# Performance work log

Hardware: AMD Instinct MI355X
Metric: run time of the kernel (lower is better)

Reference implementation:

```python
import jax, jax.numpy as jnp
import numpy as np

N_NODES = 100000
N_EDGES = 1600000
IN_CH, HID_CH, OUT_CH = 128, 128, 64


def _glorot(key, shape):
    lim = np.sqrt(6.0 / (shape[0] + shape[1])).astype(np.float32)
    return jax.random.uniform(key, shape, jnp.float32, -lim, lim)


def setup_inputs() -> dict:
    key = jax.random.key(0)
    ks = jax.random.split(key, 11)
    x = jax.random.normal(ks[0], (N_NODES, IN_CH), jnp.float32)
    edge_index = jax.random.randint(ks[1], (2, N_EDGES), 0, N_NODES, dtype=jnp.int64)
    dims = [(IN_CH, HID_CH), (HID_CH, HID_CH), (HID_CH, OUT_CH)]
    params = {}
    for i, (din, dout) in enumerate(dims):
        params[f"Wl{i}"] = _glorot(ks[2 + 3 * i], (din, dout))
        params[f"Wr{i}"] = _glorot(ks[3 + 3 * i], (din, dout))
        params[f"b{i}"] = jnp.zeros((dout,), jnp.float32)
    return {"x": x, "edge_index": edge_index, **params}


def _sage_conv(x, src, dst, Wl, Wr, b):
    # mean aggregation of neighbor (source) features at each destination node
    msg_sum = jax.ops.segment_sum(x[src], dst, num_segments=N_NODES)  # [N, din]
    deg = jax.ops.segment_sum(jnp.ones((src.shape[0],), x.dtype), dst,
                              num_segments=N_NODES)
    mean = msg_sum / jnp.maximum(deg, 1.0)[:, None]
    # lin_l(aggr) + lin_r(self), bias only in lin_l (PyG SAGEConv default)
    return mean @ Wl + x @ Wr + b


def reference(x, edge_index, Wl0, Wr0, b0, Wl1, Wr1, b1, Wl2, Wr2, b2):
    src, dst = edge_index[0], edge_index[1]
    h = jax.nn.relu(_sage_conv(x, src, dst, Wl0, Wr0, b0))  # dropout = identity (eval)
    h = jax.nn.relu(_sage_conv(h, src, dst, Wl1, Wr1, b1))
    out = _sage_conv(h, src, dst, Wl2, Wr2, b2)
    return out
```

## Files before the change

kernel.cpp:

```cpp
#include <hip/hip_runtime.h>
#include <stdint.h>

#define NN 100000
#define NE 1600000
#define NBUK 782
#define G 256
#define CHUNK 6250

typedef unsigned int u32;
typedef unsigned short u16;
typedef short v8s __attribute__((ext_vector_type(8)));
typedef float v4f __attribute__((ext_vector_type(4)));

union U4S8 {
    uint4 u;
    v8s s;
};

__device__ __forceinline__ float bf2f(u16 u) {
    return __uint_as_float(((u32)u) << 16);
}
__device__ __forceinline__ u16 f2bf(float f) {
    u32 u = __float_as_uint(f);
    u = u + 0x7FFFu + ((u >> 16) & 1u);
    return (u16)(u >> 16);
}
__device__ __forceinline__ float lo16(u32 u) { return __uint_as_float(u << 16); }
__device__ __forceinline__ float hi16(u32 u) {
    return __uint_as_float(u & 0xFFFF0000u);
}

__global__ void detect_kernel(const u32* __restrict__ ei,
                              const u32* __restrict__ x, int* flags) {
    __shared__ int bad64, badbf;
    int t = threadIdx.x;
    if (t == 0) { bad64 = 0; badbf = 0; }
    __syncthreads();
    if (ei[2 * t + 1] != 0u) atomicAdd(&bad64, 1);
    u32 d = x[t];
    u32 e = (d >> 7) & 0xFFu;
    if (e != 0u && (e < 96u || e > 160u)) atomicAdd(&badbf, 1);
    __syncthreads();
    if (t == 0) {
        flags[0] = (bad64 < 16) ? 1 : 0;
        flags[1] = (badbf < 16) ? 1 : 0;
    }
}

__global__ void conv_x(const void* __restrict__ x, const int* __restrict__ flags,
                       u32* __restrict__ xb) {
    int i = blockIdx.x * 256 + threadIdx.x;
    if (i >= NN * 64) return;
    u32 o;
    if (flags[1]) {
        o = ((const u32*)x)[i];
    } else {
        float2 v = ((const float2*)x)[i];
        o = ((u32)f2bf(v.y) << 16) | (u32)f2bf(v.x);
    }
    xb[i] = o;
}

__global__ void wt_prep(const void* __restrict__ Wr, const void* __restrict__ Wl,
                        const void* __restrict__ bias,
                        const int* __restrict__ flags, int cout,
                        u16* __restrict__ WT, float* __restrict__ bias_f) {
    int t = blockIdx.x * 256 + threadIdx.x;
    if (t < 256 * cout) {
        int k = t / cout, c = t % cout;
        const void* W = (k < 128) ? Wr : Wl;
        int kk = k & 127;
        float v;
        if (flags[1])
            v = bf2f(((const u16*)W)[kk * cout + c]);
        else
            v = ((const float*)W)[kk * cout + c];
        WT[c * 256 + k] = f2bf(v);
    }
    if (t < cout) {
        bias_f[t] =
            flags[1] ? bf2f(((const u16*)bias)[t]) : ((const float*)bias)[t];
    }
}

__global__ void zero_arr(int* p, int n) {
    int i = blockIdx.x * 256 + threadIdx.x;
    if (i < n) p[i] = 0;
}

__global__ __launch_bounds__(256) void p1_hist(const void* __restrict__ ei,
                                               const int* __restrict__ flags,
                                               int* __restrict__ hist) {
    __shared__ int h[NBUK];
    int g = blockIdx.x, t = threadIdx.x;
    for (int b = t; b < NBUK; b += 256) h[b] = 0;
    __syncthreads();
    int e0 = g * CHUNK;
    int e1 = e0 + CHUNK;
    const int* p = (const int*)ei;
    if (flags[0]) {
        for (int e = e0 + t; e < e1; e += 256)
            atomicAdd(&h[p[2 * (NE + e)] >> 7], 1);
    } else {
        for (int e = e0 + t; e < e1; e += 256)
            atomicAdd(&h[p[NE + e] >> 7], 1);
    }
    __syncthreads();
    for (int b = t; b < NBUK; b += 256) hist[b * G + g] = h[b];
}

__global__ void scan_block_g(const int* __restrict__ in, int* __restrict__ out,
                             int* __restrict__ bsums, int n) {
    __shared__ int sS[256];
    int t = threadIdx.x;
    int base = blockIdx.x * 1024 + t * 4;
    int c[4];
#pragma unroll
    for (int i = 0; i < 4; ++i) c[i] = (base + i < n) ? in[base + i] : 0;
    int s = c[0] + c[1] + c[2] + c[3];
    sS[t] = s;
    __syncthreads();
    for (int dlt = 1; dlt < 256; dlt <<= 1) {
        int v = (t >= dlt) ? sS[t - dlt] : 0;
        __syncthreads();
        sS[t] += v;
        __syncthreads();
    }
    int run = sS[t] - s;
    if (t == 255) bsums[blockIdx.x] = sS[255];
#pragma unroll
    for (int i = 0; i < 4; ++i) {
        if (base + i < n) out[base + i] = run;
        run += c[i];
    }
}

__global__ void scan_top_g(int* bsums, int nb) {
    __shared__ int sS[256];
    int t = threadIdx.x;
    int v = (t < nb) ? bsums[t] : 0;
    sS[t] = v;
    __syncthreads();
    for (int d = 1; d < 256; d <<= 1) {
        int u = (t >= d) ? sS[t - d] : 0;
        __syncthreads();
        sS[t] += u;
        __syncthreads();
    }
    if (t < nb) bsums[t] = sS[t] - v;
}

__global__ void scan_add_g(int* __restrict__ out, const int* __restrict__ bsums,
                           int n) {
    int i = blockIdx.x * 256 + threadIdx.x;
    if (i < n) out[i] += bsums[i >> 10];
}

__global__ __launch_bounds__(256) void p2_scatter(const void* __restrict__ ei,
                                                  const int* __restrict__ flags,
                                                  const int* __restrict__ histS,
                                                  int2* __restrict__ ebuf) {
    __shared__ int cur[NBUK];
    int g = blockIdx.x, t = threadIdx.x;
    for (int b = t; b < NBUK; b += 256) cur[b] = histS[b * G + g];
    __syncthreads();
    int e0 = g * CHUNK;
    int e1 = e0 + CHUNK;
    const int* p = (const int*)ei;
    int is64 = flags[0];
    for (int e = e0 + t; e < e1; e += 256) {
        int s, d;
        if (is64) {
            s = p[2 * e];
            d = p[2 * (NE + e)];
        } else {
            s = p[e];
            d = p[NE + e];
        }
        int pos = atomicAdd(&cur[d >> 7], 1);
        ebuf[pos] = make_int2(s, d);
    }
}

__global__ __launch_bounds__(256) void p3_build(const int* __restrict__ histS,
                                                const int2* __restrict__ ebuf,
                                                int* __restrict__ off,
                                                int* __restrict__ ssrc) {
    __shared__ int cnt[128], pref[128], cur[128];
    int b = blockIdx.x, t = threadIdx.x;
    int node0 = b << 7;
    int bs = histS[b * G];
    int be = (b == NBUK - 1) ? NE : histS[(b + 1) * G];
    if (t < 128) cnt[t] = 0;
    __syncthreads();
    for (int e = bs + t; e < be; e += 256)
        atomicAdd(&cnt[ebuf[e].y - node0], 1);
    __syncthreads();
    if (t < 128) pref[t] = cnt[t];
    __syncthreads();
    for (int d = 1; d < 128; d <<= 1) {
        int v = 0;
        if (t < 128 && t >= d) v = pref[t - d];
        __syncthreads();
        if (t < 128) pref[t] += v;
        __syncthreads();
    }
    if (t < 128) {
        int ex = pref[t] - cnt[t];
        cur[t] = ex;
        int node = node0 + t;
        if (node < NN) off[node] = bs + ex;
    }
    if (b == NBUK - 1 && t == 0) off[NN] = NE;
    __syncthreads();
    for (int e = bs + t; e < be; e += 256) {
        int2 sd = ebuf[e];
        int pos = atomicAdd(&cur[sd.y - node0], 1);
        ssrc[bs + pos] = sd.x;
    }
}

__global__ __launch_bounds__(256) void gather_mean_b(
    const u32* __restrict__ feat, const int* __restrict__ off,
    const int* __restrict__ ssrc, u32* __restrict__ meanB) {
    int node = blockIdx.x * 4 + (threadIdx.x >> 6);
    int lane = threadIdx.x & 63;
    int o0 = off[node], o1 = off[node + 1];
    int cnt = o1 - o0;
    float a0 = 0.f, a1 = 0.f;
    for (int base = 0; base < cnt; base += 64) {
        int lim = cnt - base;
        if (lim > 64) lim = 64;
        int myidx = (lane < lim) ? ssrc[o0 + base + lane] : 0;
        for (int j = 0; j < lim; j += 16) {
            u32 uu[16];
#pragma unroll
            for (int q = 0; q < 16; ++q) {
                int idx = __shfl(myidx, (j + q) & 63);
                uu[q] = feat[(size_t)idx * 64 + lane];
            }
#pragma unroll
            for (int q = 0; q < 16; ++q) {
                if (j + q < lim) {
                    a0 += lo16(uu[q]);
                    a1 += hi16(uu[q]);
                }
            }
        }
    }
    float inv = 1.0f / (float)(cnt > 0 ? cnt : 1);
    meanB[node * 64 + lane] =
        ((u32)f2bf(a1 * inv) << 16) | (u32)f2bf(a0 * inv);
}

template <int COUT, bool RELU, bool FINAL>
__global__ __launch_bounds__(256) void sage_mfma(
    const u16* __restrict__ selfB, const u16* __restrict__ meanB,
    const u16* __restrict__ WT, const float* __restrict__ bias_f,
    void* __restrict__ out, const int* __restrict__ flags) {
    constexpr int NT = COUT / 16;
    const int tid = threadIdx.x;
    const int wave = tid >> 6;
    const int lane = tid & 63;
    const int n16 = lane & 15;
    const int quad = lane >> 4;
    const int rowbase = blockIdx.x * 128 + wave * 32;
    const int bfin = flags[1];

    int ar0 = rowbase + n16;
    int ar1 = rowbase + 16 + n16;
    ar0 = (ar0 < NN) ? ar0 : (NN - 1);
    ar1 = (ar1 < NN) ? ar1 : (NN - 1);

    const u16* aS0 = selfB + (size_t)ar0 * 128 + quad * 8;
    const u16* aS1 = selfB + (size_t)ar1 * 128 + quad * 8;
    const u16* aM0 = meanB + (size_t)ar0 * 128 + quad * 8;
    const u16* aM1 = meanB + (size_t)ar1 * 128 + quad * 8;
    const u16* bp = WT + (size_t)n16 * 256 + quad * 8;

    v4f acc[2][NT];
#pragma unroll
    for (int mt = 0; mt < 2; ++mt)
#pragma unroll
        for (int nt = 0; nt < NT; ++nt) acc[mt][nt] = (v4f)(0.f);

#pragma unroll
    for (int ks = 0; ks < 8; ++ks) {
        const int ko = (ks & 3) * 32;
        U4S8 a0, a1;
        a0.u = *(const uint4*)((ks < 4 ? aS0 : aM0) + ko);
        a1.u = *(const uint4*)((ks < 4 ? aS1 : aM1) + ko);
        U4S8 b[NT];
#pragma unroll
        for (int nt = 0; nt < NT; ++nt)
            b[nt].u = *(const uint4*)(bp + nt * 16 * 256 + ks * 32);
#pragma unroll
        for (int nt = 0; nt < NT; ++nt) {
            acc[0][nt] = __builtin_amdgcn_mfma_f32_16x16x32_bf16(
                a0.s, b[nt].s, acc[0][nt], 0, 0, 0);
            acc[1][nt] = __builtin_amdgcn_mfma_f32_16x16x32_bf16(
                a1.s, b[nt].s, acc[1][nt], 0, 0, 0);
        }
    }

#pragma unroll
    for (int nt = 0; nt < NT; ++nt) {
        const int c = nt * 16 + n16;
        const float bv = bias_f[c];
#pragma unroll
        for (int mt = 0; mt < 2; ++mt) {
#pragma unroll
            for (int r = 0; r < 4; ++r) {
                int row = rowbase + mt * 16 + quad * 4 + r;
                if (row < NN) {
                    float v = acc[mt][nt][r] + bv;
                    if (RELU) v = fmaxf(v, 0.f);
                    if (FINAL && !bfin)
                        ((float*)out)[(size_t)row * COUT + c] = v;
                    else
                        ((u16*)out)[(size_t)row * COUT + c] = f2bf(v);
                }
            }
        }
    }
}

extern "C" void kernel_launch(void* const* d_in, const int* in_sizes, int n_in,
                              void* d_out, int out_size, void* d_ws,
                              size_t ws_size, hipStream_t stream) {
    const void* x = d_in[0];
    const void* ei = d_in[1];
    const void* Wl0 = d_in[2];
    const void* Wr0 = d_in[3];
    const void* b0 = d_in[4];
    const void* Wl1 = d_in[5];
    const void* Wr1 = d_in[6];
    const void* b1 = d_in[7];
    const void* Wl2 = d_in[8];
    const void* Wr2 = d_in[9];
    const void* b2 = d_in[10];

    char* ws = (char*)d_ws;
    size_t o = 0;
    auto alloc = [&](size_t bytes) {
        void* p = ws + o;
        o = (o + bytes + 511) & ~(size_t)511;
        return p;
    };
    int* flags = (int*)alloc(16);
    int* hist = (int*)alloc((size_t)NBUK * G * 4);
    int* bsums = (int*)alloc(256 * 4);
    int* off = (int*)alloc((NN + 1) * 4);
    int* ssrc = (int*)alloc((size_t)NE * 4);
    int2* ebuf = (int2*)alloc((size_t)NE * 8);
    u32* xb = (u32*)alloc((size_t)NN * 64 * 4);
    u32* meanB = (u32*)alloc((size_t)NN * 64 * 4);
    u32* h1 = (u32*)alloc((size_t)NN * 64 * 4);
    u32* h2 = (u32*)alloc((size_t)NN * 64 * 4);
    u16* WT0 = (u16*)alloc(256 * 128 * 2);
    u16* WT1 = (u16*)alloc(256 * 128 * 2);
    u16* WT2 = (u16*)alloc(256 * 64 * 2);
    float* bf0 = (float*)alloc(128 * 4);
    float* bf1 = (float*)alloc(128 * 4);
    float* bf2_ = (float*)alloc(64 * 4);

    constexpr int L = NBUK * G;
    constexpr int NBLK = (L + 1023) / 1024;
    constexpr int RB = (NN + 127) / 128;

    detect_kernel<<<1, 256, 0, stream>>>((const u32*)ei, (const u32*)x, flags);
    conv_x<<<(NN * 64 + 255) / 256, 256, 0, stream>>>(x, flags, xb);
    wt_prep<<<128, 256, 0, stream>>>(Wr0, Wl0, b0, flags, 128, WT0, bf0);
    wt_prep<<<128, 256, 0, stream>>>(Wr1, Wl1, b1, flags, 128, WT1, bf1);
    wt_prep<<<64, 256, 0, stream>>>(Wr2, Wl2, b2, flags, 64, WT2, bf2_);

    p1_hist<<<G, 256, 0, stream>>>(ei, flags, hist);
    scan_block_g<<<NBLK, 256, 0, stream>>>(hist, hist, bsums, L);
    scan_top_g<<<1, 256, 0, stream>>>(bsums, NBLK);
    scan_add_g<<<(L + 255) / 256, 256, 0, stream>>>(hist, bsums, L);
    p2_scatter<<<G, 256, 0, stream>>>(ei, flags, hist, ebuf);
    p3_build<<<NBUK, 256, 0, stream>>>(hist, ebuf, off, ssrc);

    gather_mean_b<<<NN / 4, 256, 0, stream>>>(xb, off, ssrc, meanB);
    sage_mfma<128, true, false><<<RB, 256, 0, stream>>>(
        (const u16*)xb, (const u16*)meanB, WT0, bf0, h1, flags);
    gather_mean_b<<<NN / 4, 256, 0, stream>>>(h1, off, ssrc, meanB);
    sage_mfma<128, true, false><<<RB, 256, 0, stream>>>(
        (const u16*)h1, (const u16*)meanB, WT1, bf1, h2, flags);
    gather_mean_b<<<NN / 4, 256, 0, stream>>>(h2, off, ssrc, meanB);
    sage_mfma<64, false, true><<<RB, 256, 0, stream>>>(
        (const u16*)h2, (const u16*)meanB, WT2, bf2_, d_out, flags);
}
```

Measured before the change: 498.9 us.

## Use scalar readlane gathers with zero-padded sentinel row and merge weight prep

The gather kernel now reads offsets via readfirstlane and broadcasts neighbor indices with readlane instead of shfl. This turns the per-row address into a scalar value and avoids LDS-based shuffles. Out-of-range lanes point to a padded all-zero sentinel row (index NN), so the per-element bounds check in the accumulate loop goes away. The three weight-prep launches are merged into one kernel, and conv_x zeroes the sentinel rows. In exchange, padded iterations issue extra loads of the zero row.

```diff
diff --git a/kernel.cpp b/kernel.cpp
--- a/kernel.cpp
+++ b/kernel.cpp
@@ -48,9 +48,18 @@
 }
 
 __global__ void conv_x(const void* __restrict__ x, const int* __restrict__ flags,
-                       u32* __restrict__ xb) {
+                       u32* __restrict__ xb, u32* __restrict__ h1,
+                       u32* __restrict__ h2) {
     int i = blockIdx.x * 256 + threadIdx.x;
-    if (i >= NN * 64) return;
+    if (i >= NN * 64) {
+        int p = i - NN * 64;
+        if (p < 64) {
+            xb[NN * 64 + p] = 0;
+            h1[NN * 64 + p] = 0;
+            h2[NN * 64 + p] = 0;
+        }
+        return;
+    }
     u32 o;
     if (flags[1]) {
         o = ((const u32*)x)[i];
@@ -61,11 +70,35 @@
     xb[i] = o;
 }
 
-__global__ void wt_prep(const void* __restrict__ Wr, const void* __restrict__ Wl,
-                        const void* __restrict__ bias,
-                        const int* __restrict__ flags, int cout,
-                        u16* __restrict__ WT, float* __restrict__ bias_f) {
-    int t = blockIdx.x * 256 + threadIdx.x;
+__global__ void wt_prep_all(const void* __restrict__ Wr0,
+                            const void* __restrict__ Wl0,
+                            const void* __restrict__ b0,
+                            const void* __restrict__ Wr1,
+                            const void* __restrict__ Wl1,
+                            const void* __restrict__ b1,
+                            const void* __restrict__ Wr2,
+                            const void* __restrict__ Wl2,
+                            const void* __restrict__ b2,
+                            const int* __restrict__ flags,
+                            u16* __restrict__ WT0, float* __restrict__ bf0,
+                            u16* __restrict__ WT1, float* __restrict__ bf1,
+                            u16* __restrict__ WT2, float* __restrict__ bf2_) {
+    const void* Wr;
+    const void* Wl;
+    const void* bias;
+    u16* WT;
+    float* bias_f;
+    int cout, t;
+    if (blockIdx.x < 128) {
+        Wr = Wr0; Wl = Wl0; bias = b0; WT = WT0; bias_f = bf0; cout = 128;
+        t = blockIdx.x * 256 + threadIdx.x;
+    } else if (blockIdx.x < 256) {
+        Wr = Wr1; Wl = Wl1; bias = b1; WT = WT1; bias_f = bf1; cout = 128;
+        t = (blockIdx.x - 128) * 256 + threadIdx.x;
+    } else {
+        Wr = Wr2; Wl = Wl2; bias = b2; WT = WT2; bias_f = bf2_; cout = 64;
+        t = (blockIdx.x - 256) * 256 + threadIdx.x;
+    }
     if (t < 256 * cout) {
         int k = t / cout, c = t % cout;
         const void* W = (k < 128) ? Wr : Wl;
@@ -81,11 +114,6 @@
         bias_f[t] =
             flags[1] ? bf2f(((const u16*)bias)[t]) : ((const float*)bias)[t];
     }
-}
-
-__global__ void zero_arr(int* p, int n) {
-    int i = blockIdx.x * 256 + threadIdx.x;
-    if (i < n) p[i] = 0;
 }
 
 __global__ __launch_bounds__(256) void p1_hist(const void* __restrict__ ei,
@@ -225,26 +253,26 @@
     const int* __restrict__ ssrc, u32* __restrict__ meanB) {
     int node = blockIdx.x * 4 + (threadIdx.x >> 6);
     int lane = threadIdx.x & 63;
-    int o0 = off[node], o1 = off[node + 1];
+    int o0 = __builtin_amdgcn_readfirstlane(off[node]);
+    int o1 = __builtin_amdgcn_readfirstlane(off[node + 1]);
     int cnt = o1 - o0;
     float a0 = 0.f, a1 = 0.f;
     for (int base = 0; base < cnt; base += 64) {
         int lim = cnt - base;
         if (lim > 64) lim = 64;
-        int myidx = (lane < lim) ? ssrc[o0 + base + lane] : 0;
-        for (int j = 0; j < lim; j += 16) {
+        int myidx = (lane < lim) ? ssrc[o0 + base + lane] : NN;
+        int jb = (lim + 15) & ~15;
+        for (int j = 0; j < jb; j += 16) {
             u32 uu[16];
 #pragma unroll
             for (int q = 0; q < 16; ++q) {
-                int idx = __shfl(myidx, (j + q) & 63);
-                uu[q] = feat[(size_t)idx * 64 + lane];
+                int sidx = __builtin_amdgcn_readlane(myidx, j + q);
+                uu[q] = feat[(size_t)sidx * 64 + lane];
             }
 #pragma unroll
             for (int q = 0; q < 16; ++q) {
-                if (j + q < lim) {
-                    a0 += lo16(uu[q]);
-                    a1 += hi16(uu[q]);
-                }
+                a0 += lo16(uu[q]);
+                a1 += hi16(uu[q]);
             }
         }
     }
@@ -353,10 +381,10 @@
     int* off = (int*)alloc((NN + 1) * 4);
     int* ssrc = (int*)alloc((size_t)NE * 4);
     int2* ebuf = (int2*)alloc((size_t)NE * 8);
-    u32* xb = (u32*)alloc((size_t)NN * 64 * 4);
+    u32* xb = (u32*)alloc((size_t)(NN + 1) * 64 * 4);
     u32* meanB = (u32*)alloc((size_t)NN * 64 * 4);
-    u32* h1 = (u32*)alloc((size_t)NN * 64 * 4);
-    u32* h2 = (u32*)alloc((size_t)NN * 64 * 4);
+    u32* h1 = (u32*)alloc((size_t)(NN + 1) * 64 * 4);
+    u32* h2 = (u32*)alloc((size_t)(NN + 1) * 64 * 4);
     u16* WT0 = (u16*)alloc(256 * 128 * 2);
     u16* WT1 = (u16*)alloc(256 * 128 * 2);
     u16* WT2 = (u16*)alloc(256 * 64 * 2);
@@ -369,10 +397,11 @@
     constexpr int RB = (NN + 127) / 128;
 
     detect_kernel<<<1, 256, 0, stream>>>((const u32*)ei, (const u32*)x, flags);
-    conv_x<<<(NN * 64 + 255) / 256, 256, 0, stream>>>(x, flags, xb);
-    wt_prep<<<128, 256, 0, stream>>>(Wr0, Wl0, b0, flags, 128, WT0, bf0);
-    wt_prep<<<128, 256, 0, stream>>>(Wr1, Wl1, b1, flags, 128, WT1, bf1);
-    wt_prep<<<64, 256, 0, stream>>>(Wr2, Wl2, b2, flags, 64, WT2, bf2_);
+    conv_x<<<(NN * 64 + 64 + 255) / 256, 256, 0, stream>>>(x, flags, xb, h1,
+                                                           h2);
+    wt_prep_all<<<320, 256, 0, stream>>>(Wr0, Wl0, b0, Wr1, Wl1, b1, Wr2, Wl2,
+                                         b2, flags, WT0, bf0, WT1, bf1, WT2,
+                                         bf2_);
 
     p1_hist<<<G, 256, 0, stream>>>(ei, flags, hist);
     scan_block_g<<<NBLK, 256, 0, stream>>>(hist, hist, bsums, L);
```

After: 475.2 us. 1.05x faster.
